# Performance work log

Hardware: AMD Instinct MI355X
Metric: run time of the kernel (lower is better)

## Reference

```python
import jax, jax.numpy as jnp
import numpy as np

N_ENT = 16384   # num_entities
N_REL = 50      # num relations
D = 128         # embedding dim
B = 4           # num bases
E = 262144      # num edges (avg degree 16)


def setup_inputs() -> dict:
    key = jax.random.key(0)
    k1, k2, k3, k4, k5, k6 = jax.random.split(key, 6)
    x = jax.random.normal(k1, (N_ENT, D), dtype=jnp.float32)
    bases = jax.random.normal(k2, (B, D, D), dtype=jnp.float32) * 0.05
    comps = jax.random.normal(k3, (N_REL, B), dtype=jnp.float32)
    alpha = jax.random.normal(k4, (N_REL, 1), dtype=jnp.float32)
    edge_index = jax.random.randint(k5, (2, E), 0, N_ENT, dtype=jnp.int64)
    edge_type = jax.random.randint(k6, (E,), 0, N_REL, dtype=jnp.int64)
    return {"x": x, "bases": bases, "comps": comps, "alpha": alpha,
            "edge_index": edge_index, "edge_type": edge_type}


def reference(x, bases, comps, alpha, edge_index, edge_type):
    # R-GCN basis-decomposition message passing:
    #   msg_e = (h_j @ W_{r(e)}) * alpha_{r(e)} * norm_e,  W_r = sum_b comps[r,b] * bases[b]
    #   out_i = sum_{e: row(e)=i} msg_e
    n = x.shape[0]
    row, col = edge_index[0], edge_index[1]

    # edge_norm = 1/sqrt(D_row) * 1/sqrt(D_col) with out-degree over rows
    ones = jnp.ones(row.shape, x.dtype)
    deg = jax.ops.segment_sum(ones, row, num_segments=n)
    deg_inv = jnp.where(deg > 0, jax.lax.rsqrt(jnp.maximum(deg, 1.0)), 0.0)
    norm = deg_inv[row] * deg_inv[col]               # [E]

    h_j = x[col]                                     # [E, D] gather
    c_e = comps[edge_type]                           # [E, B] gather
    # sum_b c[e,b] * (h_j[e] @ bases[b])  ==  einsum over (b,d)
    hj_b = c_e[:, :, None] * h_j[:, None, :]         # [E, B, D]
    msg = jnp.einsum('ebd,bdf->ef', hj_b, bases)     # [E, D] big GEMM
    msg = msg * alpha[edge_type] * norm[:, None]

    out = jax.ops.segment_sum(msg, row, num_segments=n)  # scatter-add to nodes
    return out
```

## Files before the change

### kernel.cpp

```cpp
#include <hip/hip_runtime.h>
#include <stdint.h>

#define NENT 16384
#define NREL 50
#define NE   262144
#define BSTR 64
#define ASTR 260
#define POISON 0xAAAAAAAAu

typedef __attribute__((ext_vector_type(8))) short short8;
typedef __attribute__((ext_vector_type(4))) float float4v;

__device__ __forceinline__ float bf2f(uint32_t u){ return __uint_as_float(u << 16); }
__device__ __forceinline__ uint32_t fpack(float a, float b){
  uint32_t ua = __float_as_uint(a), ub = __float_as_uint(b);
  ua = (ua + 0x7fffu + ((ua >> 16) & 1u)) >> 16;
  ub = (ub + 0x7fffu + ((ub >> 16) & 1u)) >> 16;
  return ua | (ub << 16);
}
__device__ __forceinline__ unsigned short f2bf(float a){
  uint32_t ua = __float_as_uint(a);
  return (unsigned short)((ua + 0x7fffu + ((ua >> 16) & 1u)) >> 16);
}
__device__ __forceinline__ float rdlane_f(float v, int j){
  return __uint_as_float((uint32_t)__builtin_amdgcn_readlane((int)__float_as_uint(v), j));
}

__global__ __launch_bounds__(256) void k_fill(
    const float* __restrict__ W, const float* __restrict__ comps,
    const float* __restrict__ alpha,
    const int* __restrict__ eidx, const int* __restrict__ etype,
    uint32_t* __restrict__ deg, float* __restrict__ acomb,
    unsigned short* __restrict__ WTf, uint32_t* __restrict__ bucket)
{
  int gid = blockIdx.x * 256 + threadIdx.x;
  int row = eidx[gid], col = eidx[NE + gid], r = etype[gid];
  uint32_t pos = atomicAdd(&deg[row], 1u) - POISON;
  if (pos < BSTR) bucket[row * BSTR + pos] = (uint32_t)col | ((uint32_t)r << 14);

  if (gid < 65536){
    int k = gid >> 7, c = gid & 127;
    int n = c >> 4, m = c & 15, kc = k >> 5, q = (k >> 3) & 3, jj = k & 7;
    WTf[(((n * 16 + kc) * 4 + q) * 16 + m) * 8 + jj] = f2bf(W[gid]);
  }
  if (gid < NREL * 4) acomb[gid] = alpha[gid >> 2] * comps[gid];
}

__global__ __launch_bounds__(256) void k_scale(
    const float* __restrict__ x, const uint32_t* __restrict__ deg,
    uint32_t* __restrict__ xbf)
{
  int gid = blockIdx.x * 256 + threadIdx.x;
  int n = gid >> 4;
  int d = (int)(deg[n] - POISON);
  float di = (d > 0) ? rsqrtf((float)d) : 0.f;
  const float4* xin = (const float4*)x + gid * 2;
  float4 p0 = xin[0], p1 = xin[1];
  uint32_t* xo = xbf + gid * 4;
  xo[0] = fpack(di * p0.x, di * p0.y); xo[1] = fpack(di * p0.z, di * p0.w);
  xo[2] = fpack(di * p1.x, di * p1.y); xo[3] = fpack(di * p1.z, di * p1.w);
}

__global__ __launch_bounds__(256) void k_fused(
    const uint32_t* __restrict__ xbf, const uint32_t* __restrict__ deg,
    const float* __restrict__ acomb, const uint32_t* __restrict__ bucket,
    const unsigned short* __restrict__ WTf, float* __restrict__ outf)
{
  __shared__ uint32_t A_lds[16 * ASTR];
  int t = threadIdx.x, lane = t & 63, wv = t >> 6;
  int row0 = blockIdx.x * 16;

  for (int rr = wv * 4; rr < wv * 4 + 4; ++rr){
    int i = row0 + rr;
    int d = (int)(deg[i] - POISON);
    uint32_t* Arow = &A_lds[rr * ASTR];
    if (d == 0){
      Arow[lane] = 0; Arow[lane+64] = 0; Arow[lane+128] = 0; Arow[lane+192] = 0;
      continue;
    }
    int de = min(d, BSTR);
    uint32_t rec = bucket[i * BSTR + min(lane, de - 1)];
    int colO = (int)(rec & 0x3FFFu) << 6;
    int rL   = (int)(rec >> 14);
    float4 ac = (lane < de) ? ((const float4*)acomb)[rL]
                            : make_float4(0.f, 0.f, 0.f, 0.f);
    float a0=0,a1=0,a2=0,a3=0,a4=0,a5=0,a6=0,a7=0;
    int rde = (de + 3) & ~3;
    for (int j = 0; j < rde; j += 4){
      #pragma unroll
      for (int jj = 0; jj < 4; ++jj){
        int   oj = __builtin_amdgcn_readlane(colO, j + jj);
        float m0 = rdlane_f(ac.x, j + jj), m1 = rdlane_f(ac.y, j + jj);
        float m2 = rdlane_f(ac.z, j + jj), m3 = rdlane_f(ac.w, j + jj);
        uint32_t hv = xbf[oj + lane];
        float h0 = bf2f(hv & 0xffffu), h1 = bf2f(hv >> 16);
        a0 += m0*h0; a1 += m0*h1;
        a2 += m1*h0; a3 += m1*h1;
        a4 += m2*h0; a5 += m2*h1;
        a6 += m3*h0; a7 += m3*h1;
      }
    }
    float di = rsqrtf((float)d);
    Arow[lane]       = fpack(di*a0, di*a1);
    Arow[lane + 64]  = fpack(di*a2, di*a3);
    Arow[lane + 128] = fpack(di*a4, di*a5);
    Arow[lane + 192] = fpack(di*a6, di*a7);
  }
  __syncthreads();

  int m16 = lane & 15, quad = lane >> 4;
  int n0 = wv * 2;
  const short8* Bf = (const short8*)WTf;
  const uint32_t* Abase = &A_lds[m16 * ASTR];
  float4v acc0 = {0.f,0.f,0.f,0.f}, acc1 = {0.f,0.f,0.f,0.f};
  #pragma unroll
  for (int kc = 0; kc < 16; ++kc){
    short8 aF = *(const short8*)&Abase[kc * 16 + quad * 4];
    short8 b0 = Bf[(n0 * 16 + kc) * 64 + lane];
    short8 b1 = Bf[((n0 + 1) * 16 + kc) * 64 + lane];
    acc0 = __builtin_amdgcn_mfma_f32_16x16x32_bf16(aF, b0, acc0, 0, 0, 0);
    acc1 = __builtin_amdgcn_mfma_f32_16x16x32_bf16(aF, b1, acc1, 0, 0, 0);
  }
  int mrow = row0 + quad * 4;
  int c0 = n0 * 16 + m16;
  #pragma unroll
  for (int r = 0; r < 4; ++r){
    outf[(mrow + r) * 128 + c0]      = acc0[r];
    outf[(mrow + r) * 128 + c0 + 16] = acc1[r];
  }
}

extern "C" void kernel_launch(void* const* d_in, const int* in_sizes, int n_in,
                              void* d_out, int out_size, void* d_ws, size_t ws_size,
                              hipStream_t stream){
  (void)in_sizes; (void)n_in; (void)out_size; (void)ws_size;
  const float* x     = (const float*)d_in[0];
  const float* bases = (const float*)d_in[1];
  const float* comps = (const float*)d_in[2];
  const float* alpha = (const float*)d_in[3];
  const int* eidx    = (const int*)d_in[4];
  const int* etype   = (const int*)d_in[5];
  char* ws = (char*)d_ws;

  uint32_t* deg    = (uint32_t*) (ws + 0);
  float*    acomb  = (float*)    (ws + (64  << 10));
  unsigned short* WTf = (unsigned short*)(ws + (128 << 10));
  uint32_t* xbf    = (uint32_t*) (ws + (512 << 10));
  uint32_t* bucket = (uint32_t*) (ws + (5u  << 20));

  k_fill <<<NE / 256, 256, 0, stream>>>(bases, comps, alpha, eidx, etype,
                                        deg, acomb, WTf, bucket);
  k_scale<<<NE / 256, 256, 0, stream>>>(x, deg, xbf);
  k_fused<<<NENT / 16, 256, 0, stream>>>(xbf, deg, acomb, bucket, WTf,
                                         (float*)d_out);
}
```

Baseline: 108.0 us.

## Merge three kernels into one persistent kernel with a grid-wide barrier

Fuses the fill, scale and aggregate/GEMM kernels into a single launch of 1024 blocks separated by a global atomic-counter barrier, removing two kernel launch gaps. The per-column degree scaling moves out of the x conversion (x is converted to bf16 unscaled) and into the per-edge coefficient, read from deg[col] in the gather phase. The barrier relies on all 1024 blocks being co-resident (launch bounds raised to 4 blocks per SM) and on the poisoned workspace counter starting at its poison value. It also adds a spin-wait and an extra random deg lookup per edge.

```diff
diff --git a/kernel.cpp b/kernel.cpp
--- a/kernel.cpp
+++ b/kernel.cpp
@@ -6,6 +6,7 @@
 #define NE   262144
 #define BSTR 64
 #define ASTR 260
+#define NBLK 1024
 #define POISON 0xAAAAAAAAu
 
 typedef __attribute__((ext_vector_type(8))) short short8;
@@ -26,48 +27,50 @@
   return __uint_as_float((uint32_t)__builtin_amdgcn_readlane((int)__float_as_uint(v), j));
 }
 
-__global__ __launch_bounds__(256) void k_fill(
-    const float* __restrict__ W, const float* __restrict__ comps,
-    const float* __restrict__ alpha,
+__global__ __launch_bounds__(256, 4) void k_all(
+    const float* __restrict__ x, const float* __restrict__ W,
+    const float* __restrict__ comps, const float* __restrict__ alpha,
     const int* __restrict__ eidx, const int* __restrict__ etype,
     uint32_t* __restrict__ deg, float* __restrict__ acomb,
-    unsigned short* __restrict__ WTf, uint32_t* __restrict__ bucket)
-{
-  int gid = blockIdx.x * 256 + threadIdx.x;
-  int row = eidx[gid], col = eidx[NE + gid], r = etype[gid];
-  uint32_t pos = atomicAdd(&deg[row], 1u) - POISON;
-  if (pos < BSTR) bucket[row * BSTR + pos] = (uint32_t)col | ((uint32_t)r << 14);
-
-  if (gid < 65536){
-    int k = gid >> 7, c = gid & 127;
-    int n = c >> 4, m = c & 15, kc = k >> 5, q = (k >> 3) & 3, jj = k & 7;
-    WTf[(((n * 16 + kc) * 4 + q) * 16 + m) * 8 + jj] = f2bf(W[gid]);
-  }
-  if (gid < NREL * 4) acomb[gid] = alpha[gid >> 2] * comps[gid];
-}
-
-__global__ __launch_bounds__(256) void k_scale(
-    const float* __restrict__ x, const uint32_t* __restrict__ deg,
-    uint32_t* __restrict__ xbf)
-{
-  int gid = blockIdx.x * 256 + threadIdx.x;
-  int n = gid >> 4;
-  int d = (int)(deg[n] - POISON);
-  float di = (d > 0) ? rsqrtf((float)d) : 0.f;
-  const float4* xin = (const float4*)x + gid * 2;
-  float4 p0 = xin[0], p1 = xin[1];
-  uint32_t* xo = xbf + gid * 4;
-  xo[0] = fpack(di * p0.x, di * p0.y); xo[1] = fpack(di * p0.z, di * p0.w);
-  xo[2] = fpack(di * p1.x, di * p1.y); xo[3] = fpack(di * p1.z, di * p1.w);
-}
-
-__global__ __launch_bounds__(256) void k_fused(
-    const uint32_t* __restrict__ xbf, const uint32_t* __restrict__ deg,
-    const float* __restrict__ acomb, const uint32_t* __restrict__ bucket,
-    const unsigned short* __restrict__ WTf, float* __restrict__ outf)
+    unsigned short* __restrict__ WTf, uint32_t* __restrict__ xbf,
+    uint32_t* __restrict__ bucket, uint32_t* __restrict__ ctr,
+    float* __restrict__ outf)
 {
   __shared__ uint32_t A_lds[16 * ASTR];
-  int t = threadIdx.x, lane = t & 63, wv = t >> 6;
+  int t = threadIdx.x;
+  int gid = blockIdx.x * 256 + t;
+
+  {
+    int row = eidx[gid], col = eidx[NE + gid], r = etype[gid];
+    uint32_t pos = atomicAdd(&deg[row], 1u) - POISON;
+    if (pos < BSTR) bucket[row * BSTR + pos] = (uint32_t)col | ((uint32_t)r << 14);
+
+    const float4* xin = (const float4*)x + gid * 2;
+    float4 p0 = xin[0], p1 = xin[1];
+    uint32_t* xo = xbf + gid * 4;
+    xo[0] = fpack(p0.x, p0.y); xo[1] = fpack(p0.z, p0.w);
+    xo[2] = fpack(p1.x, p1.y); xo[3] = fpack(p1.z, p1.w);
+
+    if (gid < 65536){
+      int k = gid >> 7, c = gid & 127;
+      int n = c >> 4, m = c & 15, kc = k >> 5, q = (k >> 3) & 3, jj = k & 7;
+      WTf[(((n * 16 + kc) * 4 + q) * 16 + m) * 8 + jj] = f2bf(W[gid]);
+    }
+    if (gid < NREL * 4) acomb[gid] = alpha[gid >> 2] * comps[gid];
+  }
+
+  __threadfence();
+  __syncthreads();
+  if (t == 0){
+    __hip_atomic_fetch_add(ctr, 1u, __ATOMIC_ACQ_REL, __HIP_MEMORY_SCOPE_AGENT);
+    while (__hip_atomic_load(ctr, __ATOMIC_ACQUIRE, __HIP_MEMORY_SCOPE_AGENT)
+           - POISON < (uint32_t)NBLK)
+      __builtin_amdgcn_s_sleep(1);
+  }
+  __syncthreads();
+  __threadfence();
+
+  int lane = t & 63, wv = t >> 6;
   int row0 = blockIdx.x * 16;
 
   for (int rr = wv * 4; rr < wv * 4 + 4; ++rr){
@@ -80,10 +83,16 @@
     }
     int de = min(d, BSTR);
     uint32_t rec = bucket[i * BSTR + min(lane, de - 1)];
-    int colO = (int)(rec & 0x3FFFu) << 6;
+    int colN = (int)(rec & 0x3FFFu);
+    int colO = colN << 6;
     int rL   = (int)(rec >> 14);
-    float4 ac = (lane < de) ? ((const float4*)acomb)[rL]
-                            : make_float4(0.f, 0.f, 0.f, 0.f);
+    int dc   = (int)(deg[colN] - POISON);
+    float dic = (dc > 0) ? rsqrtf((float)dc) : 0.f;
+    float4 ac = make_float4(0.f, 0.f, 0.f, 0.f);
+    if (lane < de){
+      float4 a = ((const float4*)acomb)[rL];
+      ac = make_float4(a.x * dic, a.y * dic, a.z * dic, a.w * dic);
+    }
     float a0=0,a1=0,a2=0,a3=0,a4=0,a5=0,a6=0,a7=0;
     int rde = (de + 3) & ~3;
     for (int j = 0; j < rde; j += 4){
@@ -145,12 +154,11 @@
   uint32_t* deg    = (uint32_t*) (ws + 0);
   float*    acomb  = (float*)    (ws + (64  << 10));
   unsigned short* WTf = (unsigned short*)(ws + (128 << 10));
+  uint32_t* ctr    = (uint32_t*) (ws + (320 << 10));
   uint32_t* xbf    = (uint32_t*) (ws + (512 << 10));
   uint32_t* bucket = (uint32_t*) (ws + (5u  << 20));
 
-  k_fill <<<NE / 256, 256, 0, stream>>>(bases, comps, alpha, eidx, etype,
-                                        deg, acomb, WTf, bucket);
-  k_scale<<<NE / 256, 256, 0, stream>>>(x, deg, xbf);
-  k_fused<<<NENT / 16, 256, 0, stream>>>(xbf, deg, acomb, bucket, WTf,
-                                         (float*)d_out);
+  k_all<<<NBLK, 256, 0, stream>>>(x, bases, comps, alpha, eidx, etype,
+                                  deg, acomb, WTf, xbf, bucket, ctr,
+                                  (float*)d_out);
 }
```

New measurement: 339.8 us. +214.7%, slower.
